# Kernel optimization log

Measured on AMD Instinct MI355X. Metric: run time of the kernel, lower is better.

Reference implementation:

```python
import jax, jax.numpy as jnp
import numpy as np
from jax import lax

K = 3            # exact neighbors per node in setup -> inner loop bound
MAX_STEPS = K + 1  # each step removes a candidate; sentinel ends the loop


def setup_inputs() -> dict:
    key = jax.random.key(0)
    ks = jax.random.split(key, 10)
    N, Fin, E, H1, H2 = 128, 512, 128, 256, 128
    nbrs = jax.random.randint(ks[0], (N, K), 0, N)
    adj = jnp.zeros((N, N), jnp.float32).at[jnp.arange(N)[:, None], nbrs].set(1.0)
    feature_origin = jax.random.normal(ks[1], (N, Fin), jnp.float32)
    labels = jax.random.randint(ks[2], (N,), 0, 7)

    def lin(k, fi, fo):
        return (jax.random.normal(k, (fi, fo), jnp.float32) / np.float32(np.sqrt(fi)))

    return {
        "adj": adj, "feature_origin": feature_origin, "labels": labels,
        "W_e": lin(ks[3], Fin, E), "b_e": jnp.zeros((E,), jnp.float32),
        "W1": lin(ks[4], 2 * E, H1), "b1": jnp.zeros((H1,), jnp.float32),
        "W2": lin(ks[5], H1, H2), "b2": jnp.zeros((H2,), jnp.float32),
        "w_lk": lin(ks[6], H2, 1), "b_lk": jnp.zeros((1,), jnp.float32),
        "w_act": lin(ks[7], H2, 2), "b_act": jnp.zeros((2,), jnp.float32),
    }


def _forward(adj, feature_origin, W_e, b_e, W1, b1, W2, b2, w_lk, b_lk, w_act, b_act):
    N = feature_origin.shape[0]
    E = W_e.shape[1]
    embed = lambda x: jax.nn.relu(x @ W_e + b_e)
    mlp = lambda s: jax.nn.relu(jax.nn.relu(s @ W1 + b1) @ W2 + b2)
    feature0 = embed(feature_origin)                      # [N, E]
    # original quirk: `if v > 0` -> node 0 (and sentinel) get a zero neighbor feature
    nonzero_row = (jnp.arange(N) > 0)[:, None]

    def node_fn(carry, i):
        feature, updated = carry
        cand = adj[i] != 0                                # remaining candidate mask
        sel = jnp.zeros((N,), bool)                       # signal_neighbor_i as mask

        def step_fn(st, _):
            feature, cand, sel, updated, done = st
            x_i = feature[i]
            nbr = jnp.where(nonzero_row, feature, 0.0)
            s = jnp.concatenate([jnp.broadcast_to(x_i, (N, E)), nbr], axis=-1)
            sentinel = jnp.concatenate([x_i, jnp.zeros_like(x_i)])[None]
            s = jnp.concatenate([s, sentinel], axis=0)    # [N+1, 2E]
            hidden = mlp(s)                               # [N+1, H2]
            lk = (hidden @ w_lk + b_lk)[:, 0]             # [N+1]
            valid = jnp.concatenate([cand, jnp.ones((1,), bool)])
            # deterministic surrogate for Categorical sampling: argmax of dist
            ut = jnp.argmax(jnp.where(valid, lk, -jnp.inf))
            is_end = ut == N
            skip = done | is_end
            utc = jnp.minimum(ut, N - 1)
            at = (jnp.argmax(hidden[utc] @ w_act + b_act) == 1).astype(feature.dtype)
            x_ut = feature_origin[utc]
            x_self = feature_origin[i]
            self_f = sel.astype(feature.dtype)
            cnt = self_f.sum()
            sel_sum = self_f @ feature_origin
            hv = (sel_sum + at * x_ut + x_self) / (cnt + at + 1.0)
            feat2 = feature.at[i].set(embed(hv)).at[utc].set(embed(x_ut))
            feature = jnp.where(skip, feature, feat2)
            upd2 = updated.at[i].set(True).at[utc].set(True)
            updated = jnp.where(skip, updated, upd2)
            sel = sel.at[utc].set(jnp.where(skip, sel[utc], (at == 1.0) | sel[utc]))
            cand = cand.at[utc].set(jnp.where(skip, cand[utc], False))
            return (feature, cand, sel, updated, skip), None

        (feature, _, _, updated, _), _ = lax.scan(
            step_fn, (feature, cand, sel, updated, jnp.array(False)),
            None, length=MAX_STEPS)
        return (feature, updated), None

    (feature, updated), _ = lax.scan(
        node_fn, (feature0, jnp.zeros((N,), bool)), jnp.arange(N))
    # embedding mirrors every write to feature; untouched rows stay zero
    return jnp.where(updated[:, None], feature, 0.0)


def reference(adj, feature_origin, labels, W_e, b_e, W1, b1, W2, b2, w_lk, b_lk, w_act, b_act):
    return _forward(adj, feature_origin, W_e, b_e, W1, b1, W2, b2,
                    w_lk, b_lk, w_act, b_act)
```

## Files before the change

### kernel.cpp

```cpp
#include <hip/hip_runtime.h>
#include <math.h>

constexpr int Nn  = 128;
constexpr int FIN = 512;
constexpr int EE  = 128;
constexpr int H1n = 256;
constexpr int H2n = 128;

__global__ void precomp1(const float* __restrict__ fo, const float* __restrict__ We,
                         const float* __restrict__ be,
                         float* __restrict__ G0, float* __restrict__ feat)
{
    const int n = blockIdx.x;
    const int j = threadIdx.x;
    float acc = 0.f;
    for (int k = 0; k < FIN; ++k)
        acc += fo[n * FIN + k] * We[k * EE + j];
    G0[n * EE + j] = acc;
    feat[n * EE + j] = fmaxf(acc + be[j], 0.f);
}

__global__ void precomp2(const float* __restrict__ G0, const float* __restrict__ be,
                         const float* __restrict__ W1,
                         float* __restrict__ BcurG)
{
    __shared__ float f[EE];
    const int n = blockIdx.x;
    const int j = threadIdx.x;
    if (j < EE) f[j] = fmaxf(G0[n * EE + j] + be[j], 0.f);
    __syncthreads();
    float acc = 0.f;
    for (int k = 0; k < EE; ++k)
        acc += f[k] * W1[(EE + k) * H1n + j];
    BcurG[n * H1n + j] = acc;
}

template<int NR>
__device__ __forceinline__ void p2b_rows(const float h1[4][H1n],
                                         const float* __restrict__ w2,
                                         float pa[4][4][H2n],
                                         const int kq, const int j)
{
    const int kb = kq * 64;
    float ac[NR];
    #pragma unroll
    for (int r = 0; r < NR; ++r) ac[r] = 0.f;
    #pragma unroll
    for (int kk = 0; kk < 64; kk += 4) {
        const float w0 = w2[kk], w1_ = w2[kk + 1], w2_ = w2[kk + 2], w3 = w2[kk + 3];
        #pragma unroll
        for (int r = 0; r < NR; ++r) {
            const float4 h = *reinterpret_cast<const float4*>(&h1[r][kb + kk]);
            ac[r] += h.x * w0 + h.y * w1_ + h.z * w2_ + h.w * w3;
        }
    }
    #pragma unroll
    for (int r = 0; r < NR; ++r) pa[kq][r][j] = ac[r];
}

__global__ __launch_bounds__(512, 1) void seqk(
    const float* __restrict__ adj,  const float* __restrict__ W1,
    const float* __restrict__ b1,   const float* __restrict__ W2,
    const float* __restrict__ b2,   const float* __restrict__ wlk,
    const float* __restrict__ blkb, const float* __restrict__ wact,
    const float* __restrict__ bact, const float* __restrict__ be,
    const float* __restrict__ G0,   const float* __restrict__ BcurG,
    float* __restrict__ feat)
{
    __shared__ float bc[Nn * H1n];
    __shared__ float h1[4][H1n];
    __shared__ float pa[4][4][H2n];
    __shared__ float u[H1n];
    __shared__ float ubi[H1n];
    __shared__ float xsh[EE], gi[EE], gsum[EE];
    __shared__ float gc[3 * EE];
    __shared__ float sbe[EE], sb1[H1n], sb2[H2n], swlk[H2n], swact[2 * H2n];
    __shared__ float rb_lk[8], rb_a0[8], rb_a1[8];
    __shared__ unsigned long long mlds[2];

    const int tid = threadIdx.x;

    float w1reg[128];
    {
        const int col = tid & 255;
        const int rbase = (tid < 256) ? 0 : EE;
        #pragma unroll
        for (int k = 0; k < 128; ++k)
            w1reg[k] = W1[(rbase + k) * H1n + col];
    }
    float w2reg[64];
    {
        const int kq = tid >> 7, j = tid & 127;
        #pragma unroll
        for (int kk = 0; kk < 64; ++kk)
            w2reg[kk] = W2[(kq * 64 + kk) * H2n + j];
    }
    #pragma unroll
    for (int q = 0; q < 16; ++q) {
        const int idx = (q * 512 + tid) * 4;
        *reinterpret_cast<float4*>(&bc[idx]) =
            *reinterpret_cast<const float4*>(&BcurG[idx]);
    }
    if (tid < EE)  sbe[tid] = be[tid];
    if (tid < H1n) sb1[tid] = b1[tid];
    if (tid < H2n) { sb2[tid] = b2[tid]; swlk[tid] = wlk[tid]; }
    if (tid < 2 * H2n) swact[tid] = wact[tid];
    const float r_blk = blkb[0], r_ba0 = bact[0], r_ba1 = bact[1];
    unsigned long long um0 = 0ULL, um1 = 0ULL;
    __syncthreads();

    for (int i = 0; i < Nn; ++i) {
        if (tid < EE) { xsh[tid] = feat[i * EE + tid]; gsum[tid] = 0.f; }
        if (tid < 32)
            *reinterpret_cast<float4*>(&gi[tid * 4]) =
                *reinterpret_cast<const float4*>(&G0[i * EE + tid * 4]);
        if (tid < Nn) {
            const bool c = adj[i * Nn + tid] != 0.f;
            const unsigned long long m = __ballot(c);
            if ((tid & 63) == 0) mlds[tid >> 6] = m;
        }
        __syncthreads();
        unsigned long long cm0 = mlds[0], cm1 = mlds[1];
        unsigned long long sel0 = 0ULL, sel1 = 0ULL;
        float cnt = 0.f;
        int xdirty = 0;

        for (int s = 0; s < 4; ++s) {
            int cl[4]; int ncand = 0;
            {
                unsigned long long m0 = cm0, m1 = cm1;
                #pragma unroll
                for (int t = 0; t < 4; ++t) {
                    int v = -1;
                    if (m0) { v = __builtin_ctzll(m0); m0 &= m0 - 1; }
                    else if (m1) { v = 64 + __builtin_ctzll(m1); m1 &= m1 - 1; }
                    cl[t] = v;
                    if (v >= 0) ++ncand;
                }
            }
            const int needb = (cl[0] == i) | (cl[1] == i) | (cl[2] == i) | (cl[3] == i);

            const int pr = tid >> 5, pf = tid & 31;
            const bool havegc = (tid < 96) && (pr < ncand);
            float4 gtmp;
            if (havegc) {
                const int v = (pr == 0) ? cl[0] : (pr == 1) ? cl[1] : cl[2];
                gtmp = *reinterpret_cast<const float4*>(&G0[v * EE + pf * 4]);
            }
            if (tid < 256 || needb) {
                float a0 = 0.f, a1 = 0.f, a2 = 0.f, a3 = 0.f;
                #pragma unroll
                for (int q = 0; q < 32; ++q) {
                    const float4 xv = *reinterpret_cast<const float4*>(&xsh[q * 4]);
                    a0 += xv.x * w1reg[q * 4 + 0];
                    a1 += xv.y * w1reg[q * 4 + 1];
                    a2 += xv.z * w1reg[q * 4 + 2];
                    a3 += xv.w * w1reg[q * 4 + 3];
                }
                const float sres = (a0 + a1) + (a2 + a3);
                if (tid < 256) u[tid] = sres; else ubi[tid - 256] = sres;
            }
            if (havegc)
                *reinterpret_cast<float4*>(&gc[pr * EE + pf * 4]) = gtmp;
            __syncthreads();

            {
                const int half = tid >> 8, k = tid & 255;
                #pragma unroll
                for (int hh = 0; hh < 2; ++hh) {
                    const int r = hh * 2 + half;
                    const int v = (half == 0) ? (hh == 0 ? cl[0] : cl[2])
                                              : (hh == 0 ? cl[1] : cl[3]);
                    if (r <= ncand) {
                        float Bv = 0.f;
                        if (r < ncand && v > 0)
                            Bv = (v == i && needb) ? ubi[k] : bc[v * H1n + k];
                        h1[r][k] = fmaxf(u[k] + Bv + sb1[k], 0.f);
                    }
                }
            }
            __syncthreads();

            {
                const int kq = tid >> 7, j = tid & 127;
                switch (ncand) {
                    case 3:  p2b_rows<4>(h1, w2reg, pa, kq, j); break;
                    case 2:  p2b_rows<3>(h1, w2reg, pa, kq, j); break;
                    case 1:  p2b_rows<2>(h1, w2reg, pa, kq, j); break;
                    default: p2b_rows<1>(h1, w2reg, pa, kq, j); break;
                }
            }
            __syncthreads();

            {
                const int r = tid >> 7, j = tid & 127;
                const float v = pa[0][r][j] + pa[1][r][j] + pa[2][r][j] + pa[3][r][j]
                                + sb2[j];
                const float hval = fmaxf(v, 0.f);
                float plk = hval * swlk[j];
                float p0  = hval * swact[2 * j];
                float p1  = hval * swact[2 * j + 1];
                #pragma unroll
                for (int off = 32; off; off >>= 1) {
                    plk += __shfl_down(plk, off);
                    p0  += __shfl_down(p0, off);
                    p1  += __shfl_down(p1, off);
                }
                if ((tid & 63) == 0) {
                    const int w = tid >> 6;
                    rb_lk[w] = plk; rb_a0[w] = p0; rb_a1[w] = p1;
                }
            }
            __syncthreads();

            float lkv[4];
            #pragma unroll
            for (int r = 0; r < 4; ++r)
                lkv[r] = rb_lk[2 * r] + rb_lk[2 * r + 1] + r_blk;
            float bv = -INFINITY; int ut = -1, rsel = -1;
            #pragma unroll
            for (int r = 0; r < 4; ++r)
                if (r < ncand && lkv[r] > bv) { bv = lkv[r]; ut = cl[r]; rsel = r; }
            const float slk = (ncand == 0) ? lkv[0] : (ncand == 1) ? lkv[1]
                            : (ncand == 2) ? lkv[2] : lkv[3];
            const bool brk = (ut < 0) || (slk > bv);
            if (brk) break;
            const float a0v = rb_a0[2 * rsel] + rb_a0[2 * rsel + 1] + r_ba0;
            const float a1v = rb_a1[2 * rsel] + rb_a1[2 * rsel + 1] + r_ba1;
            const int at = (a1v > a0v) ? 1 : 0;
            const int utc = ut;
            const bool selOld =
                ((utc < 64 ? (sel0 >> utc) : (sel1 >> (utc - 64))) & 1ULL) != 0ULL;
            const float denom = cnt + (float)at + 1.0f;
            if (at && !selOld) {
                cnt += 1.f;
                if (utc < 64) sel0 |= 1ULL << utc; else sel1 |= 1ULL << (utc - 64);
            }
            if (utc < 64) cm0 &= ~(1ULL << utc); else cm1 &= ~(1ULL << (utc - 64));
            if (i < 64) um0 |= 1ULL << i; else um1 |= 1ULL << (i - 64);
            if (utc < 64) um0 |= 1ULL << utc; else um1 |= 1ULL << (utc - 64);
            xdirty = (utc != i) ? 1 : 0;

            if (tid < EE) {
                const float g_ut = gc[rsel * EE + tid];
                const float futc = fmaxf(g_ut + sbe[tid], 0.f);
                const float z = (gsum[tid] + (float)at * g_ut + gi[tid]) / denom
                                + sbe[tid];
                float nx = fmaxf(z, 0.f);
                if (utc == i) nx = futc;
                xsh[tid] = nx;
                if (utc != i) feat[i * EE + tid] = nx;
                feat[utc * EE + tid] = futc;
                if (at && !selOld) gsum[tid] += g_ut;
            } else if (tid >= 256) {
                const int c = tid - 256;
                bc[utc * H1n + c] = BcurG[utc * H1n + c];
            }
            __syncthreads();
        }

        if (xdirty && tid >= 256) {
            const int c = tid - 256;
            float a0 = 0.f, a1 = 0.f, a2 = 0.f, a3 = 0.f;
            #pragma unroll
            for (int q = 0; q < 32; ++q) {
                const float4 xv = *reinterpret_cast<const float4*>(&xsh[q * 4]);
                a0 += xv.x * w1reg[q * 4 + 0];
                a1 += xv.y * w1reg[q * 4 + 1];
                a2 += xv.z * w1reg[q * 4 + 2];
                a3 += xv.w * w1reg[q * 4 + 3];
            }
            bc[i * H1n + c] = (a0 + a1) + (a2 + a3);
        }
        __syncthreads();
    }

    for (int idx = tid; idx < Nn * EE; idx += 512) {
        const int n = idx >> 7;
        const bool upd = ((n < 64 ? (um0 >> n) : (um1 >> (n - 64))) & 1ULL) != 0ULL;
        const float v = feat[idx];
        feat[idx] = upd ? v : 0.f;
    }
}

extern "C" void kernel_launch(void* const* d_in, const int* in_sizes, int n_in,
                              void* d_out, int out_size, void* d_ws, size_t ws_size,
                              hipStream_t stream)
{
    (void)in_sizes; (void)n_in; (void)out_size; (void)ws_size;
    const float* adj  = (const float*)d_in[0];
    const float* fo   = (const float*)d_in[1];
    const float* We   = (const float*)d_in[3];
    const float* be   = (const float*)d_in[4];
    const float* W1   = (const float*)d_in[5];
    const float* b1   = (const float*)d_in[6];
    const float* W2   = (const float*)d_in[7];
    const float* b2   = (const float*)d_in[8];
    const float* wlk  = (const float*)d_in[9];
    const float* blkb = (const float*)d_in[10];
    const float* wact = (const float*)d_in[11];
    const float* bact = (const float*)d_in[12];

    float* ws    = (float*)d_ws;
    float* G0    = ws;
    float* BcurG = ws + 16384;
    float* feat  = (float*)d_out;

    hipLaunchKernelGGL(precomp1, dim3(Nn), dim3(EE), 0, stream, fo, We, be, G0, feat);
    hipLaunchKernelGGL(precomp2, dim3(Nn), dim3(H1n), 0, stream, G0, be, W1, BcurG);
    hipLaunchKernelGGL(seqk, dim3(1), dim3(512), 0, stream,
                       adj, W1, b1, W2, b2, wlk, blkb, wact, bact, be,
                       G0, BcurG, feat);
}
```

Baseline: 2.052 ms.

## Double thread count in sequential kernel and split dot products across thread pairs

Launches the single-block sequential kernel with 1024 threads instead of 512. Each W1 dot product is split across two threads combined with a shuffle, and the W2 stage is split into 8 k-chunks reduced through shared memory. The aim is to shorten per-thread serial FMA chains on the latency-bound critical path. In exchange, the barriers now sync more waves, register budgets shrink, and the partial-sum buffer and its reduction grow.

```diff
diff --git a/kernel.cpp b/kernel.cpp
--- a/kernel.cpp
+++ b/kernel.cpp
@@ -38,15 +38,15 @@
 template<int NR>
 __device__ __forceinline__ void p2b_rows(const float h1[4][H1n],
                                          const float* __restrict__ w2,
-                                         float pa[4][4][H2n],
+                                         float pa[8][4][H2n],
                                          const int kq, const int j)
 {
-    const int kb = kq * 64;
+    const int kb = kq * 32;
     float ac[NR];
     #pragma unroll
     for (int r = 0; r < NR; ++r) ac[r] = 0.f;
     #pragma unroll
-    for (int kk = 0; kk < 64; kk += 4) {
+    for (int kk = 0; kk < 32; kk += 4) {
         const float w0 = w2[kk], w1_ = w2[kk + 1], w2_ = w2[kk + 2], w3 = w2[kk + 3];
         #pragma unroll
         for (int r = 0; r < NR; ++r) {
@@ -58,7 +58,7 @@
     for (int r = 0; r < NR; ++r) pa[kq][r][j] = ac[r];
 }
 
-__global__ __launch_bounds__(512, 1) void seqk(
+__global__ __launch_bounds__(1024, 1) void seqk(
     const float* __restrict__ adj,  const float* __restrict__ W1,
     const float* __restrict__ b1,   const float* __restrict__ W2,
     const float* __restrict__ b2,   const float* __restrict__ wlk,
@@ -69,7 +69,7 @@
 {
     __shared__ float bc[Nn * H1n];
     __shared__ float h1[4][H1n];
-    __shared__ float pa[4][4][H2n];
+    __shared__ float pa[8][4][H2n];
     __shared__ float u[H1n];
     __shared__ float ubi[H1n];
     __shared__ float xsh[EE], gi[EE], gsum[EE];
@@ -80,24 +80,29 @@
 
     const int tid = threadIdx.x;
 
-    float w1reg[128];
+    const int c2    = tid >> 1;
+    const int halfk = tid & 1;
+    const int col   = c2 & 255;
+    const int jj    = tid & 127;
+    const int kq    = tid >> 7;
+
+    float w1reg[64];
     {
-        const int col = tid & 255;
-        const int rbase = (tid < 256) ? 0 : EE;
+        const int part = (c2 >= 256) ? EE : 0;
+        const int rbase = part + halfk * 64;
         #pragma unroll
-        for (int k = 0; k < 128; ++k)
+        for (int k = 0; k < 64; ++k)
             w1reg[k] = W1[(rbase + k) * H1n + col];
     }
-    float w2reg[64];
+    float w2reg[32];
     {
-        const int kq = tid >> 7, j = tid & 127;
         #pragma unroll
-        for (int kk = 0; kk < 64; ++kk)
-            w2reg[kk] = W2[(kq * 64 + kk) * H2n + j];
+        for (int kk = 0; kk < 32; ++kk)
+            w2reg[kk] = W2[(kq * 32 + kk) * H2n + jj];
     }
     #pragma unroll
-    for (int q = 0; q < 16; ++q) {
-        const int idx = (q * 512 + tid) * 4;
+    for (int q = 0; q < 8; ++q) {
+        const int idx = (q * 1024 + tid) * 4;
         *reinterpret_cast<float4*>(&bc[idx]) =
             *reinterpret_cast<const float4*>(&BcurG[idx]);
     }
@@ -147,55 +152,52 @@
                 const int v = (pr == 0) ? cl[0] : (pr == 1) ? cl[1] : cl[2];
                 gtmp = *reinterpret_cast<const float4*>(&G0[v * EE + pf * 4]);
             }
-            if (tid < 256 || needb) {
+            if (c2 < 256 || needb) {
+                const int kb = halfk * 64;
                 float a0 = 0.f, a1 = 0.f, a2 = 0.f, a3 = 0.f;
                 #pragma unroll
-                for (int q = 0; q < 32; ++q) {
-                    const float4 xv = *reinterpret_cast<const float4*>(&xsh[q * 4]);
+                for (int q = 0; q < 16; ++q) {
+                    const float4 xv = *reinterpret_cast<const float4*>(&xsh[kb + q * 4]);
                     a0 += xv.x * w1reg[q * 4 + 0];
                     a1 += xv.y * w1reg[q * 4 + 1];
                     a2 += xv.z * w1reg[q * 4 + 2];
                     a3 += xv.w * w1reg[q * 4 + 3];
                 }
-                const float sres = (a0 + a1) + (a2 + a3);
-                if (tid < 256) u[tid] = sres; else ubi[tid - 256] = sres;
+                float sres = (a0 + a1) + (a2 + a3);
+                sres += __shfl_xor(sres, 1);
+                if (halfk == 0) {
+                    if (c2 < 256) u[c2] = sres; else ubi[col] = sres;
+                }
             }
             if (havegc)
                 *reinterpret_cast<float4*>(&gc[pr * EE + pf * 4]) = gtmp;
             __syncthreads();
 
             {
-                const int half = tid >> 8, k = tid & 255;
+                const int r = tid >> 8, k = tid & 255;
+                if (r <= ncand) {
+                    const int v = cl[r];
+                    float Bv = 0.f;
+                    if (r < ncand && v > 0)
+                        Bv = (v == i && needb) ? ubi[k] : bc[v * H1n + k];
+                    h1[r][k] = fmaxf(u[k] + Bv + sb1[k], 0.f);
+                }
+            }
+            __syncthreads();
+
+            switch (ncand) {
+                case 3:  p2b_rows<4>(h1, w2reg, pa, kq, jj); break;
+                case 2:  p2b_rows<3>(h1, w2reg, pa, kq, jj); break;
+                case 1:  p2b_rows<2>(h1, w2reg, pa, kq, jj); break;
+                default: p2b_rows<1>(h1, w2reg, pa, kq, jj); break;
+            }
+            __syncthreads();
+
+            if (tid < 512) {
+                const int r = tid >> 7, j = tid & 127;
+                float v = sb2[j];
                 #pragma unroll
-                for (int hh = 0; hh < 2; ++hh) {
-                    const int r = hh * 2 + half;
-                    const int v = (half == 0) ? (hh == 0 ? cl[0] : cl[2])
-                                              : (hh == 0 ? cl[1] : cl[3]);
-                    if (r <= ncand) {
-                        float Bv = 0.f;
-                        if (r < ncand && v > 0)
-                            Bv = (v == i && needb) ? ubi[k] : bc[v * H1n + k];
-                        h1[r][k] = fmaxf(u[k] + Bv + sb1[k], 0.f);
-                    }
-                }
-            }
-            __syncthreads();
-
-            {
-                const int kq = tid >> 7, j = tid & 127;
-                switch (ncand) {
-                    case 3:  p2b_rows<4>(h1, w2reg, pa, kq, j); break;
-                    case 2:  p2b_rows<3>(h1, w2reg, pa, kq, j); break;
-                    case 1:  p2b_rows<2>(h1, w2reg, pa, kq, j); break;
-                    default: p2b_rows<1>(h1, w2reg, pa, kq, j); break;
-                }
-            }
-            __syncthreads();
-
-            {
-                const int r = tid >> 7, j = tid & 127;
-                const float v = pa[0][r][j] + pa[1][r][j] + pa[2][r][j] + pa[3][r][j]
-                                + sb2[j];
+                for (int q = 0; q < 8; ++q) v += pa[q][r][j];
                 const float hval = fmaxf(v, 0.f);
                 float plk = hval * swlk[j];
                 float p0  = hval * swact[2 * j];
@@ -252,30 +254,32 @@
                 if (utc != i) feat[i * EE + tid] = nx;
                 feat[utc * EE + tid] = futc;
                 if (at && !selOld) gsum[tid] += g_ut;
-            } else if (tid >= 256) {
-                const int c = tid - 256;
+            } else if (tid >= 512 && tid < 512 + H1n) {
+                const int c = tid - 512;
                 bc[utc * H1n + c] = BcurG[utc * H1n + c];
             }
             __syncthreads();
         }
 
-        if (xdirty && tid >= 256) {
-            const int c = tid - 256;
+        if (xdirty && c2 >= 256) {
+            const int kb = halfk * 64;
             float a0 = 0.f, a1 = 0.f, a2 = 0.f, a3 = 0.f;
             #pragma unroll
-            for (int q = 0; q < 32; ++q) {
-                const float4 xv = *reinterpret_cast<const float4*>(&xsh[q * 4]);
+            for (int q = 0; q < 16; ++q) {
+                const float4 xv = *reinterpret_cast<const float4*>(&xsh[kb + q * 4]);
                 a0 += xv.x * w1reg[q * 4 + 0];
                 a1 += xv.y * w1reg[q * 4 + 1];
                 a2 += xv.z * w1reg[q * 4 + 2];
                 a3 += xv.w * w1reg[q * 4 + 3];
             }
-            bc[i * H1n + c] = (a0 + a1) + (a2 + a3);
+            float sres = (a0 + a1) + (a2 + a3);
+            sres += __shfl_xor(sres, 1);
+            if (halfk == 0) bc[i * H1n + col] = sres;
         }
         __syncthreads();
     }
 
-    for (int idx = tid; idx < Nn * EE; idx += 512) {
+    for (int idx = tid; idx < Nn * EE; idx += 1024) {
         const int n = idx >> 7;
         const bool upd = ((n < 64 ? (um0 >> n) : (um1 >> (n - 64))) & 1ULL) != 0ULL;
         const float v = feat[idx];
@@ -308,7 +312,7 @@
 
     hipLaunchKernelGGL(precomp1, dim3(Nn), dim3(EE), 0, stream, fo, We, be, G0, feat);
     hipLaunchKernelGGL(precomp2, dim3(Nn), dim3(H1n), 0, stream, G0, be, W1, BcurG);
-    hipLaunchKernelGGL(seqk, dim3(1), dim3(512), 0, stream,
+    hipLaunchKernelGGL(seqk, dim3(1), dim3(1024), 0, stream,
                        adj, W1, b1, W2, b2, wlk, blkb, wact, bact, be,
                        G0, BcurG, feat);
 }
```

Measured after the change: 2.118 ms. 1.03x slower.
